# Kernel optimization log

Hardware: AMD Instinct MI355X
Metric: run time of the kernel (lower is better)

Reference implementation:

```python
import jax, jax.numpy as jnp
import numpy as np

N_HEADS = 16
D_EMBED = 1024
D_HEAD = D_EMBED // N_HEADS  # 64
B, L = 8, 4096


def setup_inputs() -> dict:
    key = jax.random.key(0)
    ks = jax.random.split(key, 8)
    s = 1.0 / np.sqrt(D_EMBED)  # linear-layer-ish init scale
    x = jax.random.normal(ks[0], (B, L, D_EMBED), dtype=jnp.float32)
    mask = jnp.ones((B, L), dtype=bool)
    Wq = jax.random.normal(ks[1], (D_EMBED, D_EMBED), dtype=jnp.float32) * s
    bq = jnp.zeros((D_EMBED,), dtype=jnp.float32)
    Wk = jax.random.normal(ks[2], (D_EMBED, D_EMBED), dtype=jnp.float32) * s
    bk = jnp.zeros((D_EMBED,), dtype=jnp.float32)
    Wv = jax.random.normal(ks[3], (D_EMBED, N_HEADS), dtype=jnp.float32) * s
    bv = jnp.zeros((N_HEADS,), dtype=jnp.float32)
    return {"x": x, "mask": mask, "Wq": Wq, "bq": bq, "Wk": Wk, "bk": bk, "Wv": Wv, "bv": bv}


def reference(x, mask, Wq, bq, Wk, bk, Wv, bv):
    # Projections. q,k: [B, H, L, Dh]; v: [B, H, L] (value head-dim is 1).
    q = (x @ Wq + bq).reshape(B, L, N_HEADS, D_HEAD).transpose(0, 2, 1, 3)
    k = (x @ Wk + bk).reshape(B, L, N_HEADS, D_HEAD).transpose(0, 2, 1, 3)
    v = (x @ Wv + bv).transpose(0, 2, 1)  # [B, H, L]
    # scores @ value == Q @ (K^T V) / sqrt(Dh) by linearity (value head-dim 1),
    # so the L x L score matrix is never materialized.
    ktv = jnp.einsum("bhld,bhl->bhd", k, v)               # [B, H, Dh]
    z = jnp.einsum("bhld,bhd->bhl", q, ktv) / np.sqrt(D_HEAD)  # [B, H, L]
    # GumbelSigmoid in deterministic (eval) mode: plain sigmoid of the logits.
    p_attn = jax.nn.sigmoid(z)
    # masked_fill(~mask.unsqueeze(1), 0.0); dropout is identity in eval mode.
    p_attn = jnp.where(mask[:, None, :], p_attn, 0.0)
    return p_attn
```

## Files before the change

### kernel.cpp

```cpp
#include <hip/hip_runtime.h>
#include <hip/hip_bf16.h>
#include <math.h>

#define BATCH 8
#define LTOT 4096
#define DEMB 1024
#define NH 16
#define DH 64
#define CHUNKS 32
#define RPB 128

#define WS_S     0
#define WS_SV    (WS_S + BATCH*DEMB*NH)
#define WS_WQ    (WS_SV + BATCH*NH)
#define WS_C     (WS_WQ + BATCH*DEMB*NH)
#define WS_SPART (WS_C + BATCH*NH)
#define WS_NEED  ((size_t)(WS_SPART + (size_t)BATCH*CHUNKS*DEMB*NH) * 4)


__global__ __launch_bounds__(1024, 4) void k1_fused(
    const float* __restrict__ x, const float* __restrict__ Wv,
    const float* __restrict__ bv, float* __restrict__ Spart,
    float* __restrict__ S, float* __restrict__ sv, int direct) {
  __shared__ float wv_sw[DEMB * NH];
  __shared__ float vt[RPB * NH];
  __shared__ float sv_red[1024];

  const int b = blockIdx.x >> 5;
  const int chunk = blockIdx.x & 31;
  const int l0 = chunk * RPB;
  const int t = threadIdx.x;

  {
    const float4* wrow = (const float4*)&Wv[(size_t)t * NH];
    const float4 r0 = wrow[0], r1 = wrow[1], r2 = wrow[2], r3 = wrow[3];
    const float vals[16] = {r0.x, r0.y, r0.z, r0.w, r1.x, r1.y, r1.z, r1.w,
                            r2.x, r2.y, r2.z, r2.w, r3.x, r3.y, r3.z, r3.w};
    const int g = t >> 2, lo = t & 3;
    #pragma unroll
    for (int h = 0; h < 16; ++h)
      wv_sw[h * DEMB + (((g ^ h) << 2) + lo)] = vals[h];
  }
  __syncthreads();

  {
    const int h = t & 15;
    const int rp = t >> 4;
    const float4* xA = (const float4*)(x + ((size_t)b * LTOT + l0 + 2 * rp) * DEMB);
    const float4* xB = xA + 256;
    const float4* wv4 = (const float4*)&wv_sw[h * DEMB];
    float cA0 = 0.f, cA1 = 0.f, cB0 = 0.f, cB1 = 0.f;
    #pragma unroll 4
    for (int g = 0; g < 128; ++g) {
      const float4 w0 = wv4[g ^ h];
      const float4 w1 = wv4[(g ^ h) + 128];
      const float4 a0 = xA[g];
      const float4 a1 = xA[g + 128];
      const float4 d0 = xB[g];
      const float4 d1 = xB[g + 128];
      cA0 += a0.x * w0.x + a0.y * w0.y + a0.z * w0.z + a0.w * w0.w;
      cA1 += a1.x * w1.x + a1.y * w1.y + a1.z * w1.z + a1.w * w1.w;
      cB0 += d0.x * w0.x + d0.y * w0.y + d0.z * w0.z + d0.w * w0.w;
      cB1 += d1.x * w1.x + d1.y * w1.y + d1.z * w1.z + d1.w * w1.w;
    }
    const float bvh = bv[h];
    const float v0 = bvh + cA0 + cA1;
    const float v1 = bvh + cB0 + cB1;
    vt[(2 * rp) * NH + h] = v0;
    vt[(2 * rp + 1) * NH + h] = v1;
    sv_red[t] = v0 + v1;
  }
  __syncthreads();

  {
    const int hg = t & 3;
    const int i4 = t >> 2;
    const float4* xb4 = (const float4*)(x + ((size_t)b * LTOT + l0) * DEMB);
    const float4* vt4 = (const float4*)vt;
    float4 accA = {0, 0, 0, 0}, accB = accA, accC = accA, accD = accA;
    float4 acc2A = {0, 0, 0, 0}, acc2B = acc2A, acc2C = acc2A, acc2D = acc2A;
    #pragma unroll 4
    for (int l = 0; l < 64; ++l) {
      const float4 xv0 = xb4[l * 256 + i4];
      const float4 vv0 = vt4[l * 4 + hg];
      const float4 xv1 = xb4[(l + 64) * 256 + i4];
      const float4 vv1 = vt4[(l + 64) * 4 + hg];
      accA.x += xv0.x * vv0.x; accA.y += xv0.x * vv0.y; accA.z += xv0.x * vv0.z; accA.w += xv0.x * vv0.w;
      accB.x += xv0.y * vv0.x; accB.y += xv0.y * vv0.y; accB.z += xv0.y * vv0.z; accB.w += xv0.y * vv0.w;
      accC.x += xv0.z * vv0.x; accC.y += xv0.z * vv0.y; accC.z += xv0.z * vv0.z; accC.w += xv0.z * vv0.w;
      accD.x += xv0.w * vv0.x; accD.y += xv0.w * vv0.y; accD.z += xv0.w * vv0.z; accD.w += xv0.w * vv0.w;
      acc2A.x += xv1.x * vv1.x; acc2A.y += xv1.x * vv1.y; acc2A.z += xv1.x * vv1.z; acc2A.w += xv1.x * vv1.w;
      acc2B.x += xv1.y * vv1.x; acc2B.y += xv1.y * vv1.y; acc2B.z += xv1.y * vv1.z; acc2B.w += xv1.y * vv1.w;
      acc2C.x += xv1.z * vv1.x; acc2C.y += xv1.z * vv1.y; acc2C.z += xv1.z * vv1.z; acc2C.w += xv1.z * vv1.w;
      acc2D.x += xv1.w * vv1.x; acc2D.y += xv1.w * vv1.y; acc2D.z += xv1.w * vv1.z; acc2D.w += xv1.w * vv1.w;
    }
    accA.x += acc2A.x; accA.y += acc2A.y; accA.z += acc2A.z; accA.w += acc2A.w;
    accB.x += acc2B.x; accB.y += acc2B.y; accB.z += acc2B.z; accB.w += acc2B.w;
    accC.x += acc2C.x; accC.y += acc2C.y; accC.z += acc2C.z; accC.w += acc2C.w;
    accD.x += acc2D.x; accD.y += acc2D.y; accD.z += acc2D.z; accD.w += acc2D.w;

    const int col0 = i4 << 2;
    if (direct) {
      float* dst = Spart + ((size_t)blockIdx.x << 14);
      *(float4*)&dst[(col0 + 0) * NH + hg * 4] = accA;
      *(float4*)&dst[(col0 + 1) * NH + hg * 4] = accB;
      *(float4*)&dst[(col0 + 2) * NH + hg * 4] = accC;
      *(float4*)&dst[(col0 + 3) * NH + hg * 4] = accD;
    } else {
      float* Sb = S + ((size_t)b << 14);
      const float4 av[4] = {accA, accB, accC, accD};
      #pragma unroll
      for (int c = 0; c < 4; ++c) {
        atomicAdd(&Sb[(col0 + c) * NH + hg * 4 + 0], av[c].x);
        atomicAdd(&Sb[(col0 + c) * NH + hg * 4 + 1], av[c].y);
        atomicAdd(&Sb[(col0 + c) * NH + hg * 4 + 2], av[c].z);
        atomicAdd(&Sb[(col0 + c) * NH + hg * 4 + 3], av[c].w);
      }
    }
  }

  if (t < 16) {
    float s = 0.f;
    #pragma unroll
    for (int rr = 0; rr < 64; ++rr) s += sv_red[rr * 16 + t];
    atomicAdd(&sv[b * NH + t], s);
  }
}

__global__ __launch_bounds__(256) void k1b_reduce(
    const float* __restrict__ Spart, float* __restrict__ S) {
  const int b = blockIdx.x >> 5;
  const int seg = blockIdx.x & 31;
  #pragma unroll
  for (int k = 0; k < 2; ++k) {
    const int idx = seg * 512 + k * 256 + threadIdx.x;
    float s = 0.f;
    #pragma unroll 8
    for (int c = 0; c < CHUNKS; ++c)
      s += Spart[((size_t)(b * CHUNKS + c) << 14) + idx];
    S[((size_t)b << 14) + idx] = s;
  }
}

__global__ __launch_bounds__(1024) void k2_ktv_wq(
    const float* __restrict__ Wq, const float* __restrict__ bq,
    const float* __restrict__ Wk, const float* __restrict__ bk,
    const float* __restrict__ S, const float* __restrict__ sv,
    float* __restrict__ wq_sw, float* __restrict__ cvec) {
  __shared__ float part[16][DH];
  __shared__ float ktv[DH];
  const int b = blockIdx.x >> 4;
  const int h = blockIdx.x & 15;
  const int t = threadIdx.x;
  const float* Sb = S + ((size_t)b << 14);

  const int d = t & 63, seg = t >> 6;
  float p = 0.f;
  #pragma unroll 4
  for (int i = seg * 64; i < seg * 64 + 64; ++i)
    p += Wk[(size_t)i * DEMB + h * DH + d] * Sb[i * NH + h];
  part[seg][d] = p;
  __syncthreads();
  if (t < 64) {
    float s = 0.f;
    #pragma unroll
    for (int k = 0; k < 16; ++k) s += part[k][t];
    s += bk[h * DH + t] * sv[b * NH + h];
    ktv[t] = s;
  }
  __syncthreads();

  {
    const int i = t;
    const float* wrow = &Wq[(size_t)i * DEMB + h * DH];
    float s0 = 0.f, s1 = 0.f;
    #pragma unroll
    for (int dd = 0; dd < DH; dd += 8) {
      const float4 w4 = *(const float4*)&wrow[dd];
      const float4 w5 = *(const float4*)&wrow[dd + 4];
      s0 += w4.x * ktv[dd] + w4.y * ktv[dd + 1] + w4.z * ktv[dd + 2] + w4.w * ktv[dd + 3];
      s1 += w5.x * ktv[dd + 4] + w5.y * ktv[dd + 5] + w5.z * ktv[dd + 6] + w5.w * ktv[dd + 7];
    }
    wq_sw[(size_t)b * DEMB * NH + h * DEMB + ((((i >> 2) ^ h) << 2) + (i & 3))] = s0 + s1;
  }
  if (t == 0) {
    float s = 0.f;
    for (int dd = 0; dd < DH; ++dd) s += bq[h * DH + dd] * ktv[dd];
    cvec[b * NH + h] = s;
  }
}

__global__ __launch_bounds__(1024, 4) void k3_z_sigmoid(
    const float* __restrict__ x, const int* __restrict__ mask,
    const float* __restrict__ wq_sw_g, const float* __restrict__ cvec,
    float* __restrict__ out) {
  __shared__ float wq_sw[DEMB * NH];
  __shared__ float c_lds[NH];

  const int b = blockIdx.x >> 5;
  const int chunk = blockIdx.x & 31;
  const int l0 = chunk * RPB;
  const int t = threadIdx.x;

  const float4* src = (const float4*)(wq_sw_g + (size_t)b * DEMB * NH);
  float4* dst = (float4*)wq_sw;
  #pragma unroll
  for (int j = t; j < DEMB * NH / 4; j += 1024) dst[j] = src[j];
  if (t < 16) c_lds[t] = cvec[b * NH + t];
  __syncthreads();

  const int h = t & 15;
  const int rp = t >> 4;
  const int l = l0 + 2 * rp;
  const float4* xA = (const float4*)(x + ((size_t)b * LTOT + l) * DEMB);
  const float4* xB = xA + 256;
  const float4* wq4 = (const float4*)&wq_sw[h * DEMB];
  float cA0 = 0.f, cA1 = 0.f, cB0 = 0.f, cB1 = 0.f;
  #pragma unroll 4
  for (int g = 0; g < 128; ++g) {
    const float4 w0 = wq4[g ^ h];
    const float4 w1 = wq4[(g ^ h) + 128];
    const float4 a0 = xA[g];
    const float4 a1 = xA[g + 128];
    const float4 d0 = xB[g];
    const float4 d1 = xB[g + 128];
    cA0 += a0.x * w0.x + a0.y * w0.y + a0.z * w0.z + a0.w * w0.w;
    cA1 += a1.x * w1.x + a1.y * w1.y + a1.z * w1.z + a1.w * w1.w;
    cB0 += d0.x * w0.x + d0.y * w0.y + d0.z * w0.z + d0.w * w0.w;
    cB1 += d1.x * w1.x + d1.y * w1.y + d1.z * w1.z + d1.w * w1.w;
  }
  const float cb = c_lds[h];
  const float z0 = (cb + cA0 + cA1) * 0.125f;
  const float z1 = (cb + cB0 + cB1) * 0.125f;
  float p0 = 1.f / (1.f + __expf(-z0));
  float p1 = 1.f / (1.f + __expf(-z1));
  if (mask[b * LTOT + l] == 0) p0 = 0.f;
  if (mask[b * LTOT + l + 1] == 0) p1 = 0.f;
  float* orow = out + ((size_t)(b * NH + h)) * LTOT;
  orow[l] = p0;
  orow[l + 1] = p1;
}

extern "C" void kernel_launch(void* const* d_in, const int* in_sizes, int n_in,
                              void* d_out, int out_size, void* d_ws, size_t ws_size,
                              hipStream_t stream) {
  const float* x  = (const float*)d_in[0];
  const int* mask = (const int*)d_in[1];
  const float* Wq = (const float*)d_in[2];
  const float* bq = (const float*)d_in[3];
  const float* Wk = (const float*)d_in[4];
  const float* bk = (const float*)d_in[5];
  const float* Wv = (const float*)d_in[6];
  const float* bv = (const float*)d_in[7];
  float* out = (float*)d_out;
  float* ws = (float*)d_ws;

  float* S      = ws + WS_S;
  float* sv     = ws + WS_SV;
  float* wq_sw  = ws + WS_WQ;
  float* cvec   = ws + WS_C;
  float* Spart  = ws + WS_SPART;

  const int direct = (ws_size >= WS_NEED) ? 1 : 0;

  hipMemsetAsync(sv, 0, BATCH * NH * sizeof(float), stream);
  if (!direct) hipMemsetAsync(S, 0, (size_t)BATCH * DEMB * NH * sizeof(float), stream);

  k1_fused<<<dim3(BATCH * CHUNKS), dim3(1024), 0, stream>>>(x, Wv, bv, Spart, S, sv, direct);
  if (direct)
    k1b_reduce<<<dim3(BATCH * CHUNKS), dim3(256), 0, stream>>>(Spart, S);
  k2_ktv_wq<<<dim3(BATCH * NH), dim3(1024), 0, stream>>>(Wq, bq, Wk, bk, S, sv, wq_sw, cvec);
  k3_z_sigmoid<<<dim3(BATCH * CHUNKS), dim3(1024), 0, stream>>>(x, mask, wq_sw, cvec, out);
}
```

Before: 375.4 us.

## Transpose S and weight layouts to head-major and remap threads to rows

Stores the Wv, Wq-derived and S intermediates head-major ([h][i]) instead of XOR-swizzled or interleaved, and remaps the thread-to-(head,row) assignment so each wave covers 8 heads by 32 row pairs. The intent is cheaper, contiguous LDS and global accesses: broadcast-friendly weight reads, coalesced k2 reads of S, and float2 output stores. The K^T V-style accumulation in k1 now loops over all 128 rows with four head accumulators per thread. The risk is new LDS bank conflicts where the swizzle was removed, and lower per-thread ILP in the S accumulation loop.

```diff
diff --git a/kernel.cpp b/kernel.cpp
--- a/kernel.cpp
+++ b/kernel.cpp
@@ -22,8 +22,8 @@
     const float* __restrict__ x, const float* __restrict__ Wv,
     const float* __restrict__ bv, float* __restrict__ Spart,
     float* __restrict__ S, float* __restrict__ sv, int direct) {
-  __shared__ float wv_sw[DEMB * NH];
-  __shared__ float vt[RPB * NH];
+  __shared__ float wvt[NH * DEMB];
+  __shared__ float vth[NH * RPB];
   __shared__ float sv_red[1024];
 
   const int b = blockIdx.x >> 5;
@@ -36,24 +36,23 @@
     const float4 r0 = wrow[0], r1 = wrow[1], r2 = wrow[2], r3 = wrow[3];
     const float vals[16] = {r0.x, r0.y, r0.z, r0.w, r1.x, r1.y, r1.z, r1.w,
                             r2.x, r2.y, r2.z, r2.w, r3.x, r3.y, r3.z, r3.w};
-    const int g = t >> 2, lo = t & 3;
-    #pragma unroll
-    for (int h = 0; h < 16; ++h)
-      wv_sw[h * DEMB + (((g ^ h) << 2) + lo)] = vals[h];
-  }
-  __syncthreads();
-
-  {
-    const int h = t & 15;
-    const int rp = t >> 4;
+    #pragma unroll
+    for (int h = 0; h < 16; ++h) wvt[h * DEMB + t] = vals[h];
+  }
+  __syncthreads();
+
+  {
+    const int w = t >> 6, lane = t & 63;
+    const int h = ((w & 7) << 1) | (lane & 1);
+    const int rp = ((w >> 3) << 5) | (lane >> 1);
     const float4* xA = (const float4*)(x + ((size_t)b * LTOT + l0 + 2 * rp) * DEMB);
     const float4* xB = xA + 256;
-    const float4* wv4 = (const float4*)&wv_sw[h * DEMB];
+    const float4* wv4 = (const float4*)&wvt[h * DEMB];
     float cA0 = 0.f, cA1 = 0.f, cB0 = 0.f, cB1 = 0.f;
     #pragma unroll 4
     for (int g = 0; g < 128; ++g) {
-      const float4 w0 = wv4[g ^ h];
-      const float4 w1 = wv4[(g ^ h) + 128];
+      const float4 w0 = wv4[g];
+      const float4 w1 = wv4[g + 128];
       const float4 a0 = xA[g];
       const float4 a1 = xA[g + 128];
       const float4 d0 = xB[g];
@@ -66,64 +65,57 @@
     const float bvh = bv[h];
     const float v0 = bvh + cA0 + cA1;
     const float v1 = bvh + cB0 + cB1;
-    vt[(2 * rp) * NH + h] = v0;
-    vt[(2 * rp + 1) * NH + h] = v1;
+    *(float2*)&vth[h * RPB + 2 * rp] = make_float2(v0, v1);
     sv_red[t] = v0 + v1;
   }
   __syncthreads();
 
   {
-    const int hg = t & 3;
-    const int i4 = t >> 2;
+    const int hg = t >> 8;
+    const int i4 = t & 255;
     const float4* xb4 = (const float4*)(x + ((size_t)b * LTOT + l0) * DEMB);
-    const float4* vt4 = (const float4*)vt;
-    float4 accA = {0, 0, 0, 0}, accB = accA, accC = accA, accD = accA;
-    float4 acc2A = {0, 0, 0, 0}, acc2B = acc2A, acc2C = acc2A, acc2D = acc2A;
+    float4 acc0 = {0, 0, 0, 0}, acc1 = acc0, acc2 = acc0, acc3 = acc0;
     #pragma unroll 4
-    for (int l = 0; l < 64; ++l) {
-      const float4 xv0 = xb4[l * 256 + i4];
-      const float4 vv0 = vt4[l * 4 + hg];
-      const float4 xv1 = xb4[(l + 64) * 256 + i4];
-      const float4 vv1 = vt4[(l + 64) * 4 + hg];
-      accA.x += xv0.x * vv0.x; accA.y += xv0.x * vv0.y; accA.z += xv0.x * vv0.z; accA.w += xv0.x * vv0.w;
-      accB.x += xv0.y * vv0.x; accB.y += xv0.y * vv0.y; accB.z += xv0.y * vv0.z; accB.w += xv0.y * vv0.w;
-      accC.x += xv0.z * vv0.x; accC.y += xv0.z * vv0.y; accC.z += xv0.z * vv0.z; accC.w += xv0.z * vv0.w;
-      accD.x += xv0.w * vv0.x; accD.y += xv0.w * vv0.y; accD.z += xv0.w * vv0.z; accD.w += xv0.w * vv0.w;
-      acc2A.x += xv1.x * vv1.x; acc2A.y += xv1.x * vv1.y; acc2A.z += xv1.x * vv1.z; acc2A.w += xv1.x * vv1.w;
-      acc2B.x += xv1.y * vv1.x; acc2B.y += xv1.y * vv1.y; acc2B.z += xv1.y * vv1.z; acc2B.w += xv1.y * vv1.w;
-      acc2C.x += xv1.z * vv1.x; acc2C.y += xv1.z * vv1.y; acc2C.z += xv1.z * vv1.z; acc2C.w += xv1.z * vv1.w;
-      acc2D.x += xv1.w * vv1.x; acc2D.y += xv1.w * vv1.y; acc2D.z += xv1.w * vv1.z; acc2D.w += xv1.w * vv1.w;
-    }
-    accA.x += acc2A.x; accA.y += acc2A.y; accA.z += acc2A.z; accA.w += acc2A.w;
-    accB.x += acc2B.x; accB.y += acc2B.y; accB.z += acc2B.z; accB.w += acc2B.w;
-    accC.x += acc2C.x; accC.y += acc2C.y; accC.z += acc2C.z; accC.w += acc2C.w;
-    accD.x += acc2D.x; accD.y += acc2D.y; accD.z += acc2D.z; accD.w += acc2D.w;
-
-    const int col0 = i4 << 2;
+    for (int l = 0; l < RPB; ++l) {
+      const float4 xv = xb4[l * 256 + i4];
+      const float v0 = vth[(4 * hg + 0) * RPB + l];
+      const float v1 = vth[(4 * hg + 1) * RPB + l];
+      const float v2 = vth[(4 * hg + 2) * RPB + l];
+      const float v3 = vth[(4 * hg + 3) * RPB + l];
+      acc0.x += xv.x * v0; acc0.y += xv.y * v0; acc0.z += xv.z * v0; acc0.w += xv.w * v0;
+      acc1.x += xv.x * v1; acc1.y += xv.y * v1; acc1.z += xv.z * v1; acc1.w += xv.w * v1;
+      acc2.x += xv.x * v2; acc2.y += xv.y * v2; acc2.z += xv.z * v2; acc2.w += xv.w * v2;
+      acc3.x += xv.x * v3; acc3.y += xv.y * v3; acc3.z += xv.z * v3; acc3.w += xv.w * v3;
+    }
     if (direct) {
       float* dst = Spart + ((size_t)blockIdx.x << 14);
-      *(float4*)&dst[(col0 + 0) * NH + hg * 4] = accA;
-      *(float4*)&dst[(col0 + 1) * NH + hg * 4] = accB;
-      *(float4*)&dst[(col0 + 2) * NH + hg * 4] = accC;
-      *(float4*)&dst[(col0 + 3) * NH + hg * 4] = accD;
+      *(float4*)&dst[(4 * hg + 0) * DEMB + 4 * i4] = acc0;
+      *(float4*)&dst[(4 * hg + 1) * DEMB + 4 * i4] = acc1;
+      *(float4*)&dst[(4 * hg + 2) * DEMB + 4 * i4] = acc2;
+      *(float4*)&dst[(4 * hg + 3) * DEMB + 4 * i4] = acc3;
     } else {
       float* Sb = S + ((size_t)b << 14);
-      const float4 av[4] = {accA, accB, accC, accD};
+      const float4 av[4] = {acc0, acc1, acc2, acc3};
       #pragma unroll
-      for (int c = 0; c < 4; ++c) {
-        atomicAdd(&Sb[(col0 + c) * NH + hg * 4 + 0], av[c].x);
-        atomicAdd(&Sb[(col0 + c) * NH + hg * 4 + 1], av[c].y);
-        atomicAdd(&Sb[(col0 + c) * NH + hg * 4 + 2], av[c].z);
-        atomicAdd(&Sb[(col0 + c) * NH + hg * 4 + 3], av[c].w);
+      for (int j = 0; j < 4; ++j) {
+        atomicAdd(&Sb[(4 * hg + j) * DEMB + 4 * i4 + 0], av[j].x);
+        atomicAdd(&Sb[(4 * hg + j) * DEMB + 4 * i4 + 1], av[j].y);
+        atomicAdd(&Sb[(4 * hg + j) * DEMB + 4 * i4 + 2], av[j].z);
+        atomicAdd(&Sb[(4 * hg + j) * DEMB + 4 * i4 + 3], av[j].w);
       }
     }
   }
 
   if (t < 16) {
-    float s = 0.f;
-    #pragma unroll
-    for (int rr = 0; rr < 64; ++rr) s += sv_red[rr * 16 + t];
-    atomicAdd(&sv[b * NH + t], s);
+    const int h = t;
+    float s = 0.f;
+    #pragma unroll
+    for (int w2 = 0; w2 < 2; ++w2) {
+      const int base = (((h >> 1) + 8 * w2) << 6) + (h & 1);
+      #pragma unroll
+      for (int j = 0; j < 32; ++j) s += sv_red[base + 2 * j];
+    }
+    atomicAdd(&sv[b * NH + h], s);
   }
 }
 
@@ -146,19 +138,19 @@
     const float* __restrict__ Wq, const float* __restrict__ bq,
     const float* __restrict__ Wk, const float* __restrict__ bk,
     const float* __restrict__ S, const float* __restrict__ sv,
-    float* __restrict__ wq_sw, float* __restrict__ cvec) {
+    float* __restrict__ wqt, float* __restrict__ cvec) {
   __shared__ float part[16][DH];
   __shared__ float ktv[DH];
   const int b = blockIdx.x >> 4;
   const int h = blockIdx.x & 15;
   const int t = threadIdx.x;
-  const float* Sb = S + ((size_t)b << 14);
+  const float* Sth = S + ((size_t)b << 14) + h * DEMB;
 
   const int d = t & 63, seg = t >> 6;
   float p = 0.f;
   #pragma unroll 4
   for (int i = seg * 64; i < seg * 64 + 64; ++i)
-    p += Wk[(size_t)i * DEMB + h * DH + d] * Sb[i * NH + h];
+    p += Wk[(size_t)i * DEMB + h * DH + d] * Sth[i];
   part[seg][d] = p;
   __syncthreads();
   if (t < 64) {
@@ -181,7 +173,7 @@
       s0 += w4.x * ktv[dd] + w4.y * ktv[dd + 1] + w4.z * ktv[dd + 2] + w4.w * ktv[dd + 3];
       s1 += w5.x * ktv[dd + 4] + w5.y * ktv[dd + 5] + w5.z * ktv[dd + 6] + w5.w * ktv[dd + 7];
     }
-    wq_sw[(size_t)b * DEMB * NH + h * DEMB + ((((i >> 2) ^ h) << 2) + (i & 3))] = s0 + s1;
+    wqt[((size_t)b << 14) + h * DEMB + i] = s0 + s1;
   }
   if (t == 0) {
     float s = 0.f;
@@ -192,9 +184,9 @@
 
 __global__ __launch_bounds__(1024, 4) void k3_z_sigmoid(
     const float* __restrict__ x, const int* __restrict__ mask,
-    const float* __restrict__ wq_sw_g, const float* __restrict__ cvec,
+    const float* __restrict__ wqt_g, const float* __restrict__ cvec,
     float* __restrict__ out) {
-  __shared__ float wq_sw[DEMB * NH];
+  __shared__ float wqt[NH * DEMB];
   __shared__ float c_lds[NH];
 
   const int b = blockIdx.x >> 5;
@@ -202,24 +194,25 @@
   const int l0 = chunk * RPB;
   const int t = threadIdx.x;
 
-  const float4* src = (const float4*)(wq_sw_g + (size_t)b * DEMB * NH);
-  float4* dst = (float4*)wq_sw;
+  const float4* src = (const float4*)(wqt_g + ((size_t)b << 14));
+  float4* dst = (float4*)wqt;
   #pragma unroll
   for (int j = t; j < DEMB * NH / 4; j += 1024) dst[j] = src[j];
   if (t < 16) c_lds[t] = cvec[b * NH + t];
   __syncthreads();
 
-  const int h = t & 15;
-  const int rp = t >> 4;
+  const int w = t >> 6, lane = t & 63;
+  const int h = ((w & 7) << 1) | (lane & 1);
+  const int rp = ((w >> 3) << 5) | (lane >> 1);
   const int l = l0 + 2 * rp;
   const float4* xA = (const float4*)(x + ((size_t)b * LTOT + l) * DEMB);
   const float4* xB = xA + 256;
-  const float4* wq4 = (const float4*)&wq_sw[h * DEMB];
+  const float4* wq4 = (const float4*)&wqt[h * DEMB];
   float cA0 = 0.f, cA1 = 0.f, cB0 = 0.f, cB1 = 0.f;
   #pragma unroll 4
   for (int g = 0; g < 128; ++g) {
-    const float4 w0 = wq4[g ^ h];
-    const float4 w1 = wq4[(g ^ h) + 128];
+    const float4 w0 = wq4[g];
+    const float4 w1 = wq4[g + 128];
     const float4 a0 = xA[g];
     const float4 a1 = xA[g + 128];
     const float4 d0 = xB[g];
@@ -237,8 +230,7 @@
   if (mask[b * LTOT + l] == 0) p0 = 0.f;
   if (mask[b * LTOT + l + 1] == 0) p1 = 0.f;
   float* orow = out + ((size_t)(b * NH + h)) * LTOT;
-  orow[l] = p0;
-  orow[l + 1] = p1;
+  *(float2*)&orow[l] = make_float2(p0, p1);
 }
 
 extern "C" void kernel_launch(void* const* d_in, const int* in_sizes, int n_in,
@@ -255,20 +247,20 @@
   float* out = (float*)d_out;
   float* ws = (float*)d_ws;
 
-  float* S      = ws + WS_S;
+  float* St     = ws + WS_S;
   float* sv     = ws + WS_SV;
-  float* wq_sw  = ws + WS_WQ;
+  float* wqt    = ws + WS_WQ;
   float* cvec   = ws + WS_C;
   float* Spart  = ws + WS_SPART;
 
   const int direct = (ws_size >= WS_NEED) ? 1 : 0;
 
   hipMemsetAsync(sv, 0, BATCH * NH * sizeof(float), stream);
-  if (!direct) hipMemsetAsync(S, 0, (size_t)BATCH * DEMB * NH * sizeof(float), stream);
-
-  k1_fused<<<dim3(BATCH * CHUNKS), dim3(1024), 0, stream>>>(x, Wv, bv, Spart, S, sv, direct);
+  if (!direct) hipMemsetAsync(St, 0, (size_t)BATCH * DEMB * NH * sizeof(float), stream);
+
+  k1_fused<<<dim3(BATCH * CHUNKS), dim3(1024), 0, stream>>>(x, Wv, bv, Spart, St, sv, direct);
   if (direct)
-    k1b_reduce<<<dim3(BATCH * CHUNKS), dim3(256), 0, stream>>>(Spart, S);
-  k2_ktv_wq<<<dim3(BATCH * NH), dim3(1024), 0, stream>>>(Wq, bq, Wk, bk, S, sv, wq_sw, cvec);
-  k3_z_sigmoid<<<dim3(BATCH * CHUNKS), dim3(1024), 0, stream>>>(x, mask, wq_sw, cvec, out);
-}
+    k1b_reduce<<<dim3(BATCH * CHUNKS), dim3(256), 0, stream>>>(Spart, St);
+  k2_ktv_wq<<<dim3(BATCH * NH), dim3(1024), 0, stream>>>(Wq, bq, Wk, bk, St, sv, wqt, cvec);
+  k3_z_sigmoid<<<dim3(BATCH * CHUNKS), dim3(1024), 0, stream>>>(x, mask, wqt, cvec, out);
+}
```

New measurement: 499.9 us. 33.2% more time.
